# Kernel tuning notes

Measured on AMD Instinct MI355X. Metric: run time of the kernel, lower is better.

Reference implementation:

```python
import jax, jax.numpy as jnp
import numpy as np

NUM_ITERATIONS = 3
EPS = 1e-12  # matches torch F.normalize default eps


def setup_inputs() -> dict:
    key = jax.random.key(0)
    k1, k2 = jax.random.split(key)
    B, IN_CAPS, IN_LEN = 64, 1152, 8
    OUT_CAPS, OUT_LEN = 64, 16
    x = jax.random.normal(k1, (B, IN_CAPS, IN_LEN), dtype=jnp.float32)
    # xavier_uniform over (out_caps, out_len, in_len): fan_in=in_len, fan_out=out_len
    limit = float(np.sqrt(6.0 / (IN_LEN + OUT_LEN)))
    weight = jax.random.uniform(k2, (OUT_CAPS, OUT_LEN, IN_LEN), dtype=jnp.float32,
                                minval=-limit, maxval=limit)
    return {"x": x, "weight": weight}


def reference(x, weight):
    # priors[b,o,n,l] = sum_i weight[o,l,i] * x[b,n,i]  -> [B, out_caps, in_caps, out_len]
    priors = jnp.einsum('oli,bni->bonl', weight, x)
    # k-means routing, similarity='dot', squash=False (module defaults)
    out = jnp.mean(priors, axis=-2, keepdims=True)  # [B, O, 1, L] initial centroid
    probs = None
    for _ in range(NUM_ITERATIONS):
        norm = jnp.linalg.norm(out, axis=-1, keepdims=True)
        out_n = out / jnp.maximum(norm, EPS)  # F.normalize(output, dim=-1)
        logits = jnp.sum(priors * out_n, axis=-1, keepdims=True)  # [B, O, N, 1]
        probs = jax.nn.softmax(logits, axis=-2)  # softmax over in_capsules
        out = jnp.sum(probs * priors, axis=-2, keepdims=True)  # [B, O, 1, L]
    # squash=False -> return raw centroid
    return out.squeeze(-2), probs.squeeze(-1)  # [B, O, L], [B, O, N]
```

## Files before the change

kernel.cpp:

```cpp
#include <hip/hip_runtime.h>
#include <math.h>


#define NCAPS 1152
#define ILEN  8
#define OCAPS 64
#define OLEN  16
#define T     256
#define NWAVE 4
#define TPW   18
#define NITER 3
#define OG    8
#define XT_PITCH 1156
#define E_PITCH  1160

typedef __attribute__((ext_vector_type(8))) short short8;
typedef __attribute__((ext_vector_type(4))) float f32x4;

__device__ __forceinline__ unsigned f2bf_u(float f) {
    unsigned u = __builtin_bit_cast(unsigned, f);
    return (u + 0x7FFFu + ((u >> 16) & 1u)) >> 16;
}
__device__ __forceinline__ unsigned pack2(float a, float b) {
    return f2bf_u(a) | (f2bf_u(b) << 16);
}
__device__ __forceinline__ float bf2f(unsigned h) {
    return __builtin_bit_cast(float, h << 16);
}
__device__ __forceinline__ short8 s8_from(unsigned a, unsigned b, unsigned c, unsigned d) {
    uint4 t = make_uint4(a, b, c, d);
    return __builtin_bit_cast(short8, t);
}

template<int CTRL>
__device__ __forceinline__ float dpp_add(float x) {
    int xi = __builtin_bit_cast(int, x);
    int r  = __builtin_amdgcn_update_dpp(0, xi, CTRL, 0xf, 0xf, true);
    return x + __builtin_bit_cast(float, r);
}
__device__ __forceinline__ float wave_sum63(float v) {
    v = dpp_add<0x111>(v);
    v = dpp_add<0x112>(v);
    v = dpp_add<0x114>(v);
    v = dpp_add<0x118>(v);
    v = dpp_add<0x142>(v);
    v = dpp_add<0x143>(v);
    return v;
}
__device__ __forceinline__ float allsum16(float v) {
    v = dpp_add<0xB1>(v);
    v = dpp_add<0x4E>(v);
    v = dpp_add<0x124>(v);
    v = dpp_add<0x128>(v);
    return v;
}

__global__ __launch_bounds__(T, 2) void caps_kernel(const float* __restrict__ x,
                                                    const float* __restrict__ w,
                                                    float* __restrict__ dout,
                                                    int probs_base) {
    const int tid  = threadIdx.x;
    const int lane = tid & 63;
    const int wid  = tid >> 6;
    const int l16  = lane & 15;
    const int quad = lane >> 4;
    const bool q0  = (quad == 0);
    const int b  = blockIdx.x >> 3;
    const int og = blockIdx.x & 7;

    __shared__ __align__(16) unsigned short xA[NCAPS][ILEN];
    __shared__ __align__(16) unsigned short xaugT[10 * XT_PITCH];
    __shared__ __align__(16) unsigned short Yl[OLEN][16];
    __shared__ __align__(16) float Wl[OG][OLEN][ILEN];
    __shared__ __align__(16) float Scmb[NWAVE][OLEN][17];
    __shared__ __align__(16) unsigned short eL[OG * E_PITCH];
    __shared__ float ZL[OG];

    ((float4*)&Wl[0][0][0])[tid] = ((const float4*)(w + (size_t)og * OG * OLEN * ILEN))[tid];
    if (tid < 128) ((unsigned*)&Yl[0][0])[tid] = 0;

    float acc0 = 0.f, acc1 = 0.f, acc2 = 0.f, acc3 = 0.f;
    float acc4 = 0.f, acc5 = 0.f, acc6 = 0.f, acc7 = 0.f;
    const float4* xs = (const float4*)(x + (size_t)b * NCAPS * ILEN);
    #pragma unroll
    for (int p = 0; p < 5; ++p) {
        const int row = p * T + tid;
        if (row < NCAPS) {
            float4 x0 = xs[row * 2], x1 = xs[row * 2 + 1];
            acc0 += x0.x; acc1 += x0.y; acc2 += x0.z; acc3 += x0.w;
            acc4 += x1.x; acc5 += x1.y; acc6 += x1.z; acc7 += x1.w;
            unsigned h0 = f2bf_u(x0.x), h1 = f2bf_u(x0.y), h2 = f2bf_u(x0.z), h3 = f2bf_u(x0.w);
            unsigned h4 = f2bf_u(x1.x), h5 = f2bf_u(x1.y), h6 = f2bf_u(x1.z), h7 = f2bf_u(x1.w);
            *(uint4*)&xA[row][0] = make_uint4(h0 | (h1 << 16), h2 | (h3 << 16),
                                              h4 | (h5 << 16), h6 | (h7 << 16));
            xaugT[0 * XT_PITCH + row] = (unsigned short)h0;
            xaugT[1 * XT_PITCH + row] = (unsigned short)h1;
            xaugT[2 * XT_PITCH + row] = (unsigned short)h2;
            xaugT[3 * XT_PITCH + row] = (unsigned short)h3;
            xaugT[4 * XT_PITCH + row] = (unsigned short)h4;
            xaugT[5 * XT_PITCH + row] = (unsigned short)h5;
            xaugT[6 * XT_PITCH + row] = (unsigned short)h6;
            xaugT[7 * XT_PITCH + row] = (unsigned short)h7;
            xaugT[8 * XT_PITCH + row] = 0x3F80;
        }
    }
    for (int idx = tid; idx < XT_PITCH; idx += T) xaugT[9 * XT_PITCH + idx] = 0;

    acc0 = wave_sum63(acc0); acc1 = wave_sum63(acc1);
    acc2 = wave_sum63(acc2); acc3 = wave_sum63(acc3);
    acc4 = wave_sum63(acc4); acc5 = wave_sum63(acc5);
    acc6 = wave_sum63(acc6); acc7 = wave_sum63(acc7);
    if (lane == 63) {
        Scmb[wid][0][0] = acc0; Scmb[wid][0][1] = acc1;
        Scmb[wid][0][2] = acc2; Scmb[wid][0][3] = acc3;
        Scmb[wid][0][4] = acc4; Scmb[wid][0][5] = acc5;
        Scmb[wid][0][6] = acc6; Scmb[wid][0][7] = acc7;
    }
    __syncthreads();

    const int jr = (l16 < 9) ? l16 : 9;
    const unsigned short* xTw = xaugT + jr * XT_PITCH + wid * (TPW * 16) + 4 * quad;
    const unsigned short* xAw = &xA[wid * (TPW * 16) + l16][0];
    const short8 zs = {0, 0, 0, 0, 0, 0, 0, 0};
    const f32x4  zc = {0.f, 0.f, 0.f, 0.f};

    #pragma unroll
    for (int it = 0; it <= NITER; ++it) {
        if (it > 0) {
            short8 bL = q0 ? *(const short8*)&Yl[l16][0] : zs;
            f32x4 sacc = zc;
            #pragma unroll
            for (int tt = 0; tt < TPW; ++tt) {
                uint2 t2 = *(const uint2*)(xTw + tt * 16);
                short8 bs = s8_from(t2.x, t2.y, 0u, 0u);
                short8 aL = q0 ? *(const short8*)(xAw + tt * 128) : zs;
                f32x4 d = __builtin_amdgcn_mfma_f32_16x16x32_bf16(aL, bL, zc, 0, 0, 0);
                float e0 = __expf(d[0]), e1 = __expf(d[1]);
                float e2 = __expf(d[2]), e3 = __expf(d[3]);
                unsigned p0 = pack2(e0, e1), p1 = pack2(e2, e3);
                if (it == NITER && l16 < OG) {
                    const int n0 = wid * (TPW * 16) + tt * 16 + 4 * quad;
                    *(unsigned*)&eL[l16 * E_PITCH + n0]     = p0;
                    *(unsigned*)&eL[l16 * E_PITCH + n0 + 2] = p1;
                }
                short8 as = s8_from(p0, p1, 0u, 0u);
                sacc = __builtin_amdgcn_mfma_f32_16x16x32_bf16(as, bs, sacc, 0, 0, 0);
            }
            #pragma unroll
            for (int r = 0; r < 4; ++r) Scmb[wid][4 * quad + r][l16] = sacc[r];
            __syncthreads();
        }

        if (tid < 128) {
            const int o = tid >> 4, l = tid & 15;
            float sv[9];
            if (it == 0) {
                #pragma unroll
                for (int i = 0; i < 8; ++i) {
                    float t = Scmb[0][0][i];
                    #pragma unroll
                    for (int ww = 1; ww < NWAVE; ++ww) t += Scmb[ww][0][i];
                    sv[i] = t;
                }
                sv[8] = (float)NCAPS;
            } else {
                #pragma unroll
                for (int i = 0; i < 9; ++i) {
                    float t = Scmb[0][o][i];
                    #pragma unroll
                    for (int ww = 1; ww < NWAVE; ++ww) t += Scmb[ww][o][i];
                    sv[i] = t;
                }
            }
            const float zinv = 1.0f / sv[8];
            const float* wrow = &Wl[o][l][0];
            float outl = wrow[0] * sv[0];
            #pragma unroll
            for (int i = 1; i < ILEN; ++i) outl = fmaf(wrow[i], sv[i], outl);
            outl *= zinv;

            if (it < NITER) {
                float n2 = allsum16(outl * outl);
                const float inv = 1.0f / fmaxf(sqrtf(n2), 1e-12f);
                const float oh = outl * inv;
                #pragma unroll
                for (int i = 0; i < ILEN; ++i) {
                    float yi = allsum16(wrow[i] * oh);
                    if (l == i) Yl[o][i] = (unsigned short)f2bf_u(yi);
                }
            } else {
                dout[((size_t)(b * OCAPS + og * OG)) * OLEN + tid] = outl;
                if (l == 0) ZL[o] = zinv;
            }
        }
        __syncthreads();
    }

    #pragma unroll
    for (int o = 0; o < OG; ++o) {
        const float zi = ZL[o];
        float* pp = dout + (size_t)probs_base + (size_t)(b * OCAPS + og * OG + o) * NCAPS;
        for (int c = tid; c < NCAPS / 4; c += T) {
            uint2 t = *(const uint2*)&eL[o * E_PITCH + 4 * c];
            float4 v;
            v.x = bf2f(t.x & 0xFFFFu) * zi;
            v.y = bf2f(t.x >> 16) * zi;
            v.z = bf2f(t.y & 0xFFFFu) * zi;
            v.w = bf2f(t.y >> 16) * zi;
            ((float4*)pp)[c] = v;
        }
    }
}

extern "C" void kernel_launch(void* const* d_in, const int* in_sizes, int n_in,
                              void* d_out, int out_size, void* d_ws, size_t ws_size,
                              hipStream_t stream) {
    const float* x = (const float*)d_in[0];
    const float* w = (const float*)d_in[1];
    float* out = (float*)d_out;
    const int Bv = in_sizes[0] / (NCAPS * ILEN);
    const int nblocks = Bv * (OCAPS / OG);
    const int probs_base = Bv * OCAPS * OLEN;
    caps_kernel<<<dim3(nblocks), dim3(T), 0, stream>>>(x, w, out, probs_base);
}
```

Baseline: 77.76 us.

## Use all 16 MFMA output columns per block and alias probability buffer onto x staging

Each block now handles 16 output capsules with 8 waves instead of 8 capsules with 4 waves, so the 16-wide MFMA tiles no longer compute unused columns. This halves the number of blocks that redundantly stage and convert the same x batch and halves the exponential work. Final-iteration exp values are kept in registers and written to a shared buffer aliased onto the x staging area, which frees shared memory. The cost is more registers per thread and fewer, larger blocks (one per batch/group pair), which may reduce latency hiding.

```diff
diff --git a/kernel.cpp b/kernel.cpp
--- a/kernel.cpp
+++ b/kernel.cpp
@@ -6,11 +6,11 @@
 #define ILEN  8
 #define OCAPS 64
 #define OLEN  16
-#define T     256
-#define NWAVE 4
-#define TPW   18
+#define T     512
+#define NWAVE 8
+#define TPW   9
 #define NITER 3
-#define OG    8
+#define OG    16
 #define XT_PITCH 1156
 #define E_PITCH  1160
 
@@ -65,34 +65,33 @@
     const int l16  = lane & 15;
     const int quad = lane >> 4;
     const bool q0  = (quad == 0);
-    const int b  = blockIdx.x >> 3;
-    const int og = blockIdx.x & 7;
-
-    __shared__ __align__(16) unsigned short xA[NCAPS][ILEN];
-    __shared__ __align__(16) unsigned short xaugT[10 * XT_PITCH];
+    const int b  = blockIdx.x >> 2;
+    const int og = blockIdx.x & 3;
+
+    __shared__ __align__(16) unsigned short pool[NCAPS * ILEN + 10 * XT_PITCH];
     __shared__ __align__(16) unsigned short Yl[OLEN][16];
     __shared__ __align__(16) float Wl[OG][OLEN][ILEN];
     __shared__ __align__(16) float Scmb[NWAVE][OLEN][17];
-    __shared__ __align__(16) unsigned short eL[OG * E_PITCH];
     __shared__ float ZL[OG];
+    unsigned short* xA    = pool;
+    unsigned short* xaugT = pool + NCAPS * ILEN;
 
     ((float4*)&Wl[0][0][0])[tid] = ((const float4*)(w + (size_t)og * OG * OLEN * ILEN))[tid];
-    if (tid < 128) ((unsigned*)&Yl[0][0])[tid] = 0;
-
-    float acc0 = 0.f, acc1 = 0.f, acc2 = 0.f, acc3 = 0.f;
-    float acc4 = 0.f, acc5 = 0.f, acc6 = 0.f, acc7 = 0.f;
+
+    float a0 = 0.f, a1 = 0.f, a2 = 0.f, a3 = 0.f;
+    float a4 = 0.f, a5 = 0.f, a6 = 0.f, a7 = 0.f;
     const float4* xs = (const float4*)(x + (size_t)b * NCAPS * ILEN);
     #pragma unroll
-    for (int p = 0; p < 5; ++p) {
+    for (int p = 0; p < 3; ++p) {
         const int row = p * T + tid;
         if (row < NCAPS) {
             float4 x0 = xs[row * 2], x1 = xs[row * 2 + 1];
-            acc0 += x0.x; acc1 += x0.y; acc2 += x0.z; acc3 += x0.w;
-            acc4 += x1.x; acc5 += x1.y; acc6 += x1.z; acc7 += x1.w;
+            a0 += x0.x; a1 += x0.y; a2 += x0.z; a3 += x0.w;
+            a4 += x1.x; a5 += x1.y; a6 += x1.z; a7 += x1.w;
             unsigned h0 = f2bf_u(x0.x), h1 = f2bf_u(x0.y), h2 = f2bf_u(x0.z), h3 = f2bf_u(x0.w);
             unsigned h4 = f2bf_u(x1.x), h5 = f2bf_u(x1.y), h6 = f2bf_u(x1.z), h7 = f2bf_u(x1.w);
-            *(uint4*)&xA[row][0] = make_uint4(h0 | (h1 << 16), h2 | (h3 << 16),
-                                              h4 | (h5 << 16), h6 | (h7 << 16));
+            *(uint4*)&xA[row * ILEN] = make_uint4(h0 | (h1 << 16), h2 | (h3 << 16),
+                                                  h4 | (h5 << 16), h6 | (h7 << 16));
             xaugT[0 * XT_PITCH + row] = (unsigned short)h0;
             xaugT[1 * XT_PITCH + row] = (unsigned short)h1;
             xaugT[2 * XT_PITCH + row] = (unsigned short)h2;
@@ -106,23 +105,23 @@
     }
     for (int idx = tid; idx < XT_PITCH; idx += T) xaugT[9 * XT_PITCH + idx] = 0;
 
-    acc0 = wave_sum63(acc0); acc1 = wave_sum63(acc1);
-    acc2 = wave_sum63(acc2); acc3 = wave_sum63(acc3);
-    acc4 = wave_sum63(acc4); acc5 = wave_sum63(acc5);
-    acc6 = wave_sum63(acc6); acc7 = wave_sum63(acc7);
+    a0 = wave_sum63(a0); a1 = wave_sum63(a1); a2 = wave_sum63(a2); a3 = wave_sum63(a3);
+    a4 = wave_sum63(a4); a5 = wave_sum63(a5); a6 = wave_sum63(a6); a7 = wave_sum63(a7);
     if (lane == 63) {
-        Scmb[wid][0][0] = acc0; Scmb[wid][0][1] = acc1;
-        Scmb[wid][0][2] = acc2; Scmb[wid][0][3] = acc3;
-        Scmb[wid][0][4] = acc4; Scmb[wid][0][5] = acc5;
-        Scmb[wid][0][6] = acc6; Scmb[wid][0][7] = acc7;
+        Scmb[wid][0][0] = a0; Scmb[wid][0][1] = a1;
+        Scmb[wid][0][2] = a2; Scmb[wid][0][3] = a3;
+        Scmb[wid][0][4] = a4; Scmb[wid][0][5] = a5;
+        Scmb[wid][0][6] = a6; Scmb[wid][0][7] = a7;
     }
     __syncthreads();
 
     const int jr = (l16 < 9) ? l16 : 9;
     const unsigned short* xTw = xaugT + jr * XT_PITCH + wid * (TPW * 16) + 4 * quad;
-    const unsigned short* xAw = &xA[wid * (TPW * 16) + l16][0];
+    const unsigned short* xAw = xA + (wid * (TPW * 16) + l16) * ILEN;
     const short8 zs = {0, 0, 0, 0, 0, 0, 0, 0};
     const f32x4  zc = {0.f, 0.f, 0.f, 0.f};
+
+    unsigned st0[TPW], st1[TPW];
 
     #pragma unroll
     for (int it = 0; it <= NITER; ++it) {
@@ -138,11 +137,7 @@
                 float e0 = __expf(d[0]), e1 = __expf(d[1]);
                 float e2 = __expf(d[2]), e3 = __expf(d[3]);
                 unsigned p0 = pack2(e0, e1), p1 = pack2(e2, e3);
-                if (it == NITER && l16 < OG) {
-                    const int n0 = wid * (TPW * 16) + tt * 16 + 4 * quad;
-                    *(unsigned*)&eL[l16 * E_PITCH + n0]     = p0;
-                    *(unsigned*)&eL[l16 * E_PITCH + n0 + 2] = p1;
-                }
+                if (it == NITER) { st0[tt] = p0; st1[tt] = p1; }
                 short8 as = s8_from(p0, p1, 0u, 0u);
                 sacc = __builtin_amdgcn_mfma_f32_16x16x32_bf16(as, bs, sacc, 0, 0, 0);
             }
@@ -151,7 +146,7 @@
             __syncthreads();
         }
 
-        if (tid < 128) {
+        if (tid < 256) {
             const int o = tid >> 4, l = tid & 15;
             float sv[9];
             if (it == 0) {
@@ -189,18 +184,32 @@
                     if (l == i) Yl[o][i] = (unsigned short)f2bf_u(yi);
                 }
             } else {
-                dout[((size_t)(b * OCAPS + og * OG)) * OLEN + tid] = outl;
+                dout[(((size_t)(b * OCAPS + og * OG + o)) << 4) + l] = outl;
                 if (l == 0) ZL[o] = zinv;
             }
         }
+
+        if (it == NITER) {
+            unsigned short* eL = pool;
+            const int n0 = wid * (TPW * 16) + 4 * quad;
+            #pragma unroll
+            for (int tt = 0; tt < TPW; ++tt) {
+                *(unsigned*)&eL[l16 * E_PITCH + n0 + tt * 16]     = st0[tt];
+                *(unsigned*)&eL[l16 * E_PITCH + n0 + tt * 16 + 2] = st1[tt];
+            }
+        }
         __syncthreads();
     }
 
-    #pragma unroll
-    for (int o = 0; o < OG; ++o) {
+    {
+        const unsigned short* eL = pool;
+        const int o  = tid >> 5;
+        const int c0 = tid & 31;
         const float zi = ZL[o];
         float* pp = dout + (size_t)probs_base + (size_t)(b * OCAPS + og * OG + o) * NCAPS;
-        for (int c = tid; c < NCAPS / 4; c += T) {
+        #pragma unroll
+        for (int j = 0; j < 9; ++j) {
+            const int c = c0 + 32 * j;
             uint2 t = *(const uint2*)&eL[o * E_PITCH + 4 * c];
             float4 v;
             v.x = bf2f(t.x & 0xFFFFu) * zi;
```

Measured after the change: 72.33 us. -7.0%, faster.
